# Performance work log

Measured on AMD Instinct MI355X. Metric: run time of the kernel, lower is better.

Reference implementation:

```python
import jax, jax.numpy as jnp
import numpy as np

N_CARD = 100000
N_MERCH = 50000
E = 1000000
DIN = 64
H = 128


def setup_inputs() -> dict:
    key = jax.random.key(0)
    ks = iter(jax.random.split(key, 40))

    def nrm(shape, scale=0.05):
        return jax.random.normal(next(ks), shape, jnp.float32) * scale

    inp = {}
    inp["x_card"] = jax.random.normal(next(ks), (N_CARD, DIN), jnp.float32)
    inp["x_merchant"] = jax.random.normal(next(ks), (N_MERCH, DIN), jnp.float32)
    inp["src_cm"] = jax.random.randint(next(ks), (E,), 0, N_CARD, jnp.int32)
    inp["dst_cm"] = jax.random.randint(next(ks), (E,), 0, N_MERCH, jnp.int32)
    inp["src_mc"] = jax.random.randint(next(ks), (E,), 0, N_MERCH, jnp.int32)
    inp["dst_mc"] = jax.random.randint(next(ks), (E,), 0, N_CARD, jnp.int32)
    # SAGEConv weights per layer / edge type: lin_l (on aggregated msgs, with bias), lin_r (on dst, no bias)
    inp["Wl0_cm"] = nrm((DIN, H)); inp["bl0_cm"] = jnp.zeros((H,), jnp.float32); inp["Wr0_cm"] = nrm((DIN, H))
    inp["Wl0_mc"] = nrm((DIN, H)); inp["bl0_mc"] = jnp.zeros((H,), jnp.float32); inp["Wr0_mc"] = nrm((DIN, H))
    inp["Wl1_cm"] = nrm((H, H)); inp["bl1_cm"] = jnp.zeros((H,), jnp.float32); inp["Wr1_cm"] = nrm((H, H))
    inp["Wl1_mc"] = nrm((H, H)); inp["bl1_mc"] = jnp.zeros((H,), jnp.float32); inp["Wr1_mc"] = nrm((H, H))
    # per-node-type fraud classifiers: Linear(H, H//2) -> ReLU -> Linear(H//2, 2)
    inp["cW1_card"] = nrm((H, H // 2)); inp["cb1_card"] = jnp.zeros((H // 2,), jnp.float32)
    inp["cW2_card"] = nrm((H // 2, 2)); inp["cb2_card"] = jnp.zeros((2,), jnp.float32)
    inp["cW1_merch"] = nrm((H, H // 2)); inp["cb1_merch"] = jnp.zeros((H // 2,), jnp.float32)
    inp["cW2_merch"] = nrm((H // 2, 2)); inp["cb2_merch"] = jnp.zeros((2,), jnp.float32)
    # shared risk scorer: Linear(H, H//2) -> ReLU -> Linear(H//2, 1) -> sigmoid
    inp["rW1"] = nrm((H, H // 2)); inp["rb1"] = jnp.zeros((H // 2,), jnp.float32)
    inp["rW2"] = nrm((H // 2, 1)); inp["rb2"] = jnp.zeros((1,), jnp.float32)
    return inp


def _sage(x_src, x_dst, src, dst, Wl, bl, Wr, n_dst):
    # gather neighbor features, scatter-mean by destination, then lin_l + lin_r(x_dst)
    msg = x_src[src]                                           # [E, Din]
    agg = jax.ops.segment_sum(msg, dst, num_segments=n_dst)    # [n_dst, Din]
    cnt = jax.ops.segment_sum(jnp.ones((src.shape[0],), x_src.dtype), dst, num_segments=n_dst)
    mean = agg / jnp.maximum(cnt, 1.0)[:, None]
    return mean @ Wl + bl + x_dst @ Wr


def _mlp2(x, W1, b1, W2, b2):
    return jax.nn.relu(x @ W1 + b1) @ W2 + b2


def reference(x_card, x_merchant, src_cm, dst_cm, src_mc, dst_mc,
              Wl0_cm, bl0_cm, Wr0_cm, Wl0_mc, bl0_mc, Wr0_mc,
              Wl1_cm, bl1_cm, Wr1_cm, Wl1_mc, bl1_mc, Wr1_mc,
              cW1_card, cb1_card, cW2_card, cb2_card,
              cW1_merch, cb1_merch, cW2_merch, cb2_merch,
              rW1, rb1, rW2, rb2):
    # layer 0 (eval mode: dropout is identity)
    h_m = jax.nn.relu(_sage(x_card, x_merchant, src_cm, dst_cm, Wl0_cm, bl0_cm, Wr0_cm, N_MERCH))
    h_c = jax.nn.relu(_sage(x_merchant, x_card, src_mc, dst_mc, Wl0_mc, bl0_mc, Wr0_mc, N_CARD))
    # layer 1
    h_m2 = jax.nn.relu(_sage(h_c, h_m, src_cm, dst_cm, Wl1_cm, bl1_cm, Wr1_cm, N_MERCH))
    h_c2 = jax.nn.relu(_sage(h_m, h_c, src_mc, dst_mc, Wl1_mc, bl1_mc, Wr1_mc, N_CARD))
    # heads
    pred_c = _mlp2(h_c2, cW1_card, cb1_card, cW2_card, cb2_card)      # [N_CARD, 2]
    pred_m = _mlp2(h_m2, cW1_merch, cb1_merch, cW2_merch, cb2_merch)  # [N_MERCH, 2]
    risk_c = jax.nn.sigmoid(_mlp2(h_c2, rW1, rb1, rW2, rb2))[:, 0]    # [N_CARD]
    risk_m = jax.nn.sigmoid(_mlp2(h_m2, rW1, rb1, rW2, rb2))[:, 0]    # [N_MERCH]
    return (h_c2, h_m2, pred_c, pred_m, risk_c, risk_m)
```

## Files before the change

### kernel.cpp

```cpp
#include <hip/hip_runtime.h>


typedef unsigned short u16;
typedef unsigned int u32;
typedef short bf16x8 __attribute__((ext_vector_type(8)));
typedef float f32x4 __attribute__((ext_vector_type(4)));
typedef u16 u16x4 __attribute__((ext_vector_type(4)));
typedef u16 u16x8 __attribute__((ext_vector_type(8)));

#define CAP 64
#define LDS_PAD 8

__device__ __forceinline__ float bf2f(u16 u) {
    union { u32 i; float f; } v; v.i = ((u32)u) << 16; return v.f;
}
__device__ __forceinline__ u16 f2bf(float f) {
    union { float f; u32 i; } v; v.f = f;
    u32 i = v.i;
    return (u16)((i + 0x7FFFu + ((i >> 16) & 1u)) >> 16);
}
__device__ __forceinline__ bf16x8 cvt8(const float* p) {
    bf16x8 r;
#pragma unroll
    for (int i = 0; i < 8; ++i) r[i] = (short)f2bf(p[i]);
    return r;
}

struct PackDesc { const float* src; u16* dst; int K; int Nsrc; int ntOff; };
struct PackArgs { PackDesc d[12]; };

__global__ void __launch_bounds__(256) pack_all(PackArgs pa) {
    PackDesc pd = pa.d[blockIdx.y];
    int idx = blockIdx.x * 256 + threadIdx.x;
    int j = idx & 7;
    int lane = (idx >> 3) & 63;
    int t = idx >> 9;
    int nLocal = pd.Nsrc >> 4;
    int ntl = t % nLocal;
    int kt = t / nLocal;
    if (kt >= (pd.K >> 5)) return;
    int k = kt * 32 + ((lane >> 4) << 3) + j;
    int n = ntl * 16 + (lane & 15);
    pd.dst[(((kt * 8 + pd.ntOff + ntl) * 64) + lane) * 8 + j] = f2bf(pd.src[k * pd.Nsrc + n]);
}

__global__ void __launch_bounds__(256) build_buckets(
    const int* __restrict__ src_cm, const int* __restrict__ dst_cm,
    const int* __restrict__ src_mc, const int* __restrict__ dst_mc,
    int* __restrict__ cnt_m, u32* __restrict__ bucket_m,
    int* __restrict__ cnt_c, u16* __restrict__ bucket_c, int E)
{
    int i = blockIdx.x * 256 + threadIdx.x;
    if (i < E) {
        int d = dst_cm[i];
        int slot = atomicAdd(&cnt_m[d], 1);
        if (slot < CAP) bucket_m[(size_t)d * CAP + slot] = (u32)src_cm[i];
    } else if (i < 2 * E) {
        int j = i - E;
        int d = dst_mc[j];
        int slot = atomicAdd(&cnt_c[d], 1);
        if (slot < CAP) bucket_c[(size_t)d * CAP + slot] = (u16)src_mc[j];
    }
}

template<typename IdxT, int KF, bool SRCF, bool DSTF, bool OUTF>
__global__ void __launch_bounds__(256) sage_fused(
    const void* __restrict__ Xsrc_, const IdxT* __restrict__ adj,
    const int* __restrict__ cnt,
    const u16* __restrict__ Wlp, const void* __restrict__ Xdst_,
    const u16* __restrict__ Wrp, const float* __restrict__ bias,
    void* __restrict__ out_, int M)
{
    constexpr int NV = KF / 16;
    __shared__ alignas(16) u16 lds[4][16][128 + LDS_PAD];
    const int lane = threadIdx.x & 63;
    const int wv = threadIdx.x >> 6;
    const int m0 = (blockIdx.x * 4 + wv) * 16;
    const bool active = (m0 < M);
    const int quad = lane >> 4;
    const int l15 = lane & 15;
    const int nb = quad;
    const int fl = l15;

    if (active) {
        const float* srcF = (const float*)Xsrc_;
        const u16*   srcH = (const u16*)Xsrc_;
        for (int r = 0; r < 16; ++r) {
            int node = m0 + r;
            int c = cnt[node];
            int cc = min(c, CAP);
            int sidx = (lane < cc) ? (int)adj[(size_t)node * CAP + lane] : 0;
            float inv = 1.f / (float)max(c, 1);
            float acc0[NV], acc1[NV];
#pragma unroll
            for (int i = 0; i < NV; ++i) { acc0[i] = 0.f; acc1[i] = 0.f; }
            for (int t = 0; t < cc; t += 8) {
                int k0 = t + nb;
                int k1 = t + nb + 4;
                int s0 = __shfl(sidx, k0);
                int s1 = __shfl(sidx, k1);
                bool p0 = k0 < cc;
                bool p1 = k1 < cc;
                if constexpr (SRCF) {
                    const f32x4* q0 = (const f32x4*)(srcF + (size_t)s0 * KF + fl * NV);
                    const f32x4* q1 = (const f32x4*)(srcF + (size_t)s1 * KF + fl * NV);
                    f32x4 u0 = q0[0];
                    f32x4 u1 = q1[0];
                    if constexpr (NV == 8) {
                        f32x4 w0 = q0[1];
                        f32x4 w1 = q1[1];
#pragma unroll
                        for (int i = 0; i < 4; ++i) {
                            acc0[4 + i] += p0 ? w0[i] : 0.f;
                            acc1[4 + i] += p1 ? w1[i] : 0.f;
                        }
                    }
#pragma unroll
                    for (int i = 0; i < 4; ++i) {
                        acc0[i] += p0 ? u0[i] : 0.f;
                        acc1[i] += p1 ? u1[i] : 0.f;
                    }
                } else {
                    bf16x8 u0 = *(const bf16x8*)(srcH + (size_t)s0 * KF + fl * 8);
                    bf16x8 u1 = *(const bf16x8*)(srcH + (size_t)s1 * KF + fl * 8);
#pragma unroll
                    for (int i = 0; i < 8; ++i) {
                        acc0[i] += p0 ? bf2f((u16)u0[i]) : 0.f;
                        acc1[i] += p1 ? bf2f((u16)u1[i]) : 0.f;
                    }
                }
            }
            u16 packed[NV];
#pragma unroll
            for (int i = 0; i < NV; ++i) {
                float m = acc0[i] + acc1[i];
                m += __shfl_xor(m, 16);
                m += __shfl_xor(m, 32);
                packed[i] = f2bf(m * inv);
            }
            if (nb == 0) {
                if constexpr (NV == 8) {
                    *(u16x8*)&lds[wv][r][fl * 8] = *(const u16x8*)packed;
                } else {
                    *(u16x4*)&lds[wv][r][fl * 4] = *(const u16x4*)packed;
                }
            }
        }
    }
    __syncthreads();
    if (!active) return;

    constexpr int KT = KF >> 5;
    f32x4 acc[8];
#pragma unroll
    for (int i = 0; i < 8; ++i) acc[i] = (f32x4){0.f, 0.f, 0.f, 0.f};

#pragma unroll
    for (int kt = 0; kt < KT; ++kt) {
        bf16x8 a = *reinterpret_cast<const bf16x8*>(&lds[wv][l15][kt * 32 + quad * 8]);
#pragma unroll
        for (int nt = 0; nt < 8; ++nt) {
            bf16x8 b = *reinterpret_cast<const bf16x8*>(Wlp + (size_t)(((kt * 8 + nt) * 64 + lane) * 8));
            acc[nt] = __builtin_amdgcn_mfma_f32_16x16x32_bf16(a, b, acc[nt], 0, 0, 0);
        }
    }
#pragma unroll
    for (int kt = 0; kt < KT; ++kt) {
        bf16x8 a;
        if constexpr (DSTF) a = cvt8((const float*)Xdst_ + (size_t)(m0 + l15) * KF + kt * 32 + quad * 8);
        else                a = *reinterpret_cast<const bf16x8*>((const u16*)Xdst_ + (size_t)(m0 + l15) * KF + kt * 32 + quad * 8);
#pragma unroll
        for (int nt = 0; nt < 8; ++nt) {
            bf16x8 b = *reinterpret_cast<const bf16x8*>(Wrp + (size_t)(((kt * 8 + nt) * 64 + lane) * 8));
            acc[nt] = __builtin_amdgcn_mfma_f32_16x16x32_bf16(a, b, acc[nt], 0, 0, 0);
        }
    }
#pragma unroll
    for (int nt = 0; nt < 8; ++nt) {
        int col = nt * 16 + l15;
        float bv = bias[col];
#pragma unroll
        for (int r = 0; r < 4; ++r) {
            int row = m0 + quad * 4 + r;
            float v = fmaxf(acc[nt][r] + bv, 0.f);
            if constexpr (OUTF) ((float*)out_)[(size_t)row * 128 + col] = v;
            else                ((u16*)out_)[(size_t)row * 128 + col] = f2bf(v);
        }
    }
}

__global__ void __launch_bounds__(256) head_fused(
    const float* __restrict__ X, const u16* __restrict__ W1p,
    const float* __restrict__ b1a, const float* __restrict__ b1b,
    const float* __restrict__ cW2, const float* __restrict__ cb2,
    const float* __restrict__ rW2, const float* __restrict__ rb2,
    float* __restrict__ pred, float* __restrict__ risk, int M)
{
    __shared__ alignas(16) u16 lds[4][16][128 + LDS_PAD];
    const int lane = threadIdx.x & 63;
    const int wv = threadIdx.x >> 6;
    const int m0 = (blockIdx.x * 4 + wv) * 16;
    const bool active = (m0 < M);
    const int quad = lane >> 4;
    const int l15 = lane & 15;

    if (active) {
        f32x4 acc[8];
#pragma unroll
        for (int i = 0; i < 8; ++i) acc[i] = (f32x4){0.f, 0.f, 0.f, 0.f};
#pragma unroll
        for (int kt = 0; kt < 4; ++kt) {
            bf16x8 a = cvt8(X + (size_t)(m0 + l15) * 128 + kt * 32 + quad * 8);
#pragma unroll
            for (int nt = 0; nt < 8; ++nt) {
                bf16x8 b = *reinterpret_cast<const bf16x8*>(W1p + (size_t)(((kt * 8 + nt) * 64 + lane) * 8));
                acc[nt] = __builtin_amdgcn_mfma_f32_16x16x32_bf16(a, b, acc[nt], 0, 0, 0);
            }
        }
#pragma unroll
        for (int nt = 0; nt < 8; ++nt) {
            int col = nt * 16 + l15;
            float bv = (col < 64) ? b1a[col] : b1b[col - 64];
#pragma unroll
            for (int r = 0; r < 4; ++r) {
                float v = fmaxf(acc[nt][r] + bv, 0.f);
                lds[wv][quad * 4 + r][col] = f2bf(v);
            }
        }
    }
    __syncthreads();
    if (!active) return;

    float w0 = cW2[lane * 2 + 0];
    float w1 = cW2[lane * 2 + 1];
    float w2 = rW2[lane];
    float cb0 = cb2[0], cb1v = cb2[1], rb = rb2[0];
    for (int r = 0; r < 16; ++r) {
        float t1 = bf2f(lds[wv][r][lane]);
        float t2 = bf2f(lds[wv][r][64 + lane]);
        float s0 = t1 * w0;
        float s1 = t1 * w1;
        float s2 = t2 * w2;
        for (int off = 32; off > 0; off >>= 1) {
            s0 += __shfl_xor(s0, off);
            s1 += __shfl_xor(s1, off);
            s2 += __shfl_xor(s2, off);
        }
        if (lane == 0) {
            int row = m0 + r;
            pred[(size_t)row * 2 + 0] = s0 + cb0;
            pred[(size_t)row * 2 + 1] = s1 + cb1v;
            float z = s2 + rb;
            risk[row] = 1.f / (1.f + __expf(-z));
        }
    }
}

#define OFF_CNT_M  ((size_t)0)
#define OFF_CNT_C  ((size_t)262144)
#define OFF_BKT_M  ((size_t)1  << 20)
#define OFF_BKT_C  ((size_t)14 << 20)
#define OFF_HM     ((size_t)27 << 20)
#define OFF_PACK   ((size_t)40 << 20)

extern "C" void kernel_launch(void* const* d_in, const int* in_sizes, int n_in,
                              void* d_out, int out_size, void* d_ws, size_t ws_size,
                              hipStream_t stream)
{
    const float* x_card   = (const float*)d_in[0];
    const float* x_merch  = (const float*)d_in[1];
    const int* src_cm     = (const int*)d_in[2];
    const int* dst_cm     = (const int*)d_in[3];
    const int* src_mc     = (const int*)d_in[4];
    const int* dst_mc     = (const int*)d_in[5];
    const float* Wl0_cm   = (const float*)d_in[6];
    const float* bl0_cm   = (const float*)d_in[7];
    const float* Wr0_cm   = (const float*)d_in[8];
    const float* Wl0_mc   = (const float*)d_in[9];
    const float* bl0_mc   = (const float*)d_in[10];
    const float* Wr0_mc   = (const float*)d_in[11];
    const float* Wl1_cm   = (const float*)d_in[12];
    const float* bl1_cm   = (const float*)d_in[13];
    const float* Wr1_cm   = (const float*)d_in[14];
    const float* Wl1_mc   = (const float*)d_in[15];
    const float* bl1_mc   = (const float*)d_in[16];
    const float* Wr1_mc   = (const float*)d_in[17];
    const float* cW1_card = (const float*)d_in[18];
    const float* cb1_card = (const float*)d_in[19];
    const float* cW2_card = (const float*)d_in[20];
    const float* cb2_card = (const float*)d_in[21];
    const float* cW1_mer  = (const float*)d_in[22];
    const float* cb1_mer  = (const float*)d_in[23];
    const float* cW2_mer  = (const float*)d_in[24];
    const float* cb2_mer  = (const float*)d_in[25];
    const float* rW1      = (const float*)d_in[26];
    const float* rb1      = (const float*)d_in[27];
    const float* rW2      = (const float*)d_in[28];
    const float* rb2      = (const float*)d_in[29];

    const int nCard  = in_sizes[0] / 64;
    const int nMerch = in_sizes[1] / 64;
    const int E      = in_sizes[2];

    char* ws = (char*)d_ws;
    int* cnt_m    = (int*)(ws + OFF_CNT_M);
    int* cnt_c    = (int*)(ws + OFF_CNT_C);
    u32* bucket_m = (u32*)(ws + OFF_BKT_M);
    u16* bucket_c = (u16*)(ws + OFF_BKT_C);
    u16* h_m      = (u16*)(ws + OFF_HM);
    u16* pw       = (u16*)(ws + OFF_PACK);
    u16* pWl0_cm = pw + 0 * 16384;
    u16* pWr0_cm = pw + 1 * 16384;
    u16* pWl0_mc = pw + 2 * 16384;
    u16* pWr0_mc = pw + 3 * 16384;
    u16* pWl1_cm = pw + 4 * 16384;
    u16* pWr1_cm = pw + 5 * 16384;
    u16* pWl1_mc = pw + 6 * 16384;
    u16* pWr1_mc = pw + 7 * 16384;
    u16* pHeadC  = pw + 8 * 16384;
    u16* pHeadM  = pw + 9 * 16384;

    float* out     = (float*)d_out;
    float* o_hc2   = out;
    float* o_hm2   = o_hc2 + (size_t)nCard * 128;
    float* o_predc = o_hm2 + (size_t)nMerch * 128;
    float* o_predm = o_predc + (size_t)nCard * 2;
    float* o_riskc = o_predm + (size_t)nMerch * 2;
    float* o_riskm = o_riskc + (size_t)nCard;

    hipMemsetAsync(ws, 0, OFF_CNT_C + (size_t)nCard * sizeof(int), stream);

    PackArgs pa;
    pa.d[0]  = { Wl0_cm,   pWl0_cm,  64, 128, 0 };
    pa.d[1]  = { Wr0_cm,   pWr0_cm,  64, 128, 0 };
    pa.d[2]  = { Wl0_mc,   pWl0_mc,  64, 128, 0 };
    pa.d[3]  = { Wr0_mc,   pWr0_mc,  64, 128, 0 };
    pa.d[4]  = { Wl1_cm,   pWl1_cm, 128, 128, 0 };
    pa.d[5]  = { Wr1_cm,   pWr1_cm, 128, 128, 0 };
    pa.d[6]  = { Wl1_mc,   pWl1_mc, 128, 128, 0 };
    pa.d[7]  = { Wr1_mc,   pWr1_mc, 128, 128, 0 };
    pa.d[8]  = { cW1_card, pHeadC,  128,  64, 0 };
    pa.d[9]  = { rW1,      pHeadC,  128,  64, 4 };
    pa.d[10] = { cW1_mer,  pHeadM,  128,  64, 0 };
    pa.d[11] = { rW1,      pHeadM,  128,  64, 4 };
    pack_all<<<dim3(64, 12), 256, 0, stream>>>(pa);

    build_buckets<<<(2 * E + 255) / 256, 256, 0, stream>>>(
        src_cm, dst_cm, src_mc, dst_mc, cnt_m, bucket_m, cnt_c, bucket_c, E);

    sage_fused<u32, 64, true, true, false><<<(nMerch + 63) / 64, 256, 0, stream>>>(
        x_card, bucket_m, cnt_m, pWl0_cm, x_merch, pWr0_cm, bl0_cm, h_m, nMerch);
    sage_fused<u16, 64, true, true, true><<<(nCard + 63) / 64, 256, 0, stream>>>(
        x_merch, bucket_c, cnt_c, pWl0_mc, x_card, pWr0_mc, bl0_mc, o_hc2, nCard);

    sage_fused<u32, 128, true, false, true><<<(nMerch + 63) / 64, 256, 0, stream>>>(
        o_hc2, bucket_m, cnt_m, pWl1_cm, h_m, pWr1_cm, bl1_cm, o_hm2, nMerch);
    sage_fused<u16, 128, false, true, true><<<(nCard + 63) / 64, 256, 0, stream>>>(
        h_m, bucket_c, cnt_c, pWl1_mc, o_hc2, pWr1_mc, bl1_mc, o_hc2, nCard);

    head_fused<<<(nCard + 63) / 64, 256, 0, stream>>>(
        o_hc2, pHeadC, cb1_card, rb1, cW2_card, cb2_card, rW2, rb2, o_predc, o_riskc, nCard);
    head_fused<<<(nMerch + 63) / 64, 256, 0, stream>>>(
        o_hm2, pHeadM, cb1_mer, rb1, cW2_mer, cb2_mer, rW2, rb2, o_predm, o_riskm, nMerch);
}
```

Baseline: 660.1 us.

## Partition bucket build with LDS counters and gather from bf16 shadow copies

Bucket construction is replaced by 64 blocks, each owning a slice of destination nodes. Each block scans every edge and counts its own destinations with LDS atomics, which removes the global atomics and the counter memset. Node features and the layer-0 card output are also converted to bf16 shadow buffers, so the random neighbour gathers move half the bytes. In exchange, each block rereads the full 4 MB dst array (64 passes in total), only 64 blocks run, extra conversion kernels are added, and the shadow path depends on workspace size.

```diff
diff --git a/kernel.cpp b/kernel.cpp
--- a/kernel.cpp
+++ b/kernel.cpp
@@ -10,6 +10,7 @@
 
 #define CAP 64
 #define LDS_PAD 8
+#define NPART 32
 
 __device__ __forceinline__ float bf2f(u16 u) {
     union { u32 i; float f; } v; v.i = ((u32)u) << 16; return v.f;
@@ -44,32 +45,80 @@
     pd.dst[(((kt * 8 + pd.ntOff + ntl) * 64) + lane) * 8 + j] = f2bf(pd.src[k * pd.Nsrc + n]);
 }
 
-__global__ void __launch_bounds__(256) build_buckets(
+__global__ void __launch_bounds__(256) f32_to_bf16(
+    const float* __restrict__ a, u16* __restrict__ b, int n)
+{
+    int i = (blockIdx.x * 256 + threadIdx.x) * 4;
+    if (i >= n) return;
+    f32x4 v = *reinterpret_cast<const f32x4*>(a + i);
+    u16x4 o;
+#pragma unroll
+    for (int j = 0; j < 4; ++j) o[j] = f2bf(v[j]);
+    *reinterpret_cast<u16x4*>(b + i) = o;
+}
+
+__global__ void __launch_bounds__(256) build_buckets_part(
     const int* __restrict__ src_cm, const int* __restrict__ dst_cm,
     const int* __restrict__ src_mc, const int* __restrict__ dst_mc,
     int* __restrict__ cnt_m, u32* __restrict__ bucket_m,
-    int* __restrict__ cnt_c, u16* __restrict__ bucket_c, int E)
+    int* __restrict__ cnt_c, u16* __restrict__ bucket_c,
+    int E, int nMerch, int nCard)
 {
-    int i = blockIdx.x * 256 + threadIdx.x;
-    if (i < E) {
-        int d = dst_cm[i];
-        int slot = atomicAdd(&cnt_m[d], 1);
-        if (slot < CAP) bucket_m[(size_t)d * CAP + slot] = (u32)src_cm[i];
-    } else if (i < 2 * E) {
-        int j = i - E;
-        int d = dst_mc[j];
-        int slot = atomicAdd(&cnt_c[d], 1);
-        if (slot < CAP) bucket_c[(size_t)d * CAP + slot] = (u16)src_mc[j];
-    }
-}
-
-template<typename IdxT, int KF, bool SRCF, bool DSTF, bool OUTF>
+    __shared__ int lcnt[3136];
+    const bool dirA = blockIdx.x < NPART;
+    const int part = dirA ? blockIdx.x : blockIdx.x - NPART;
+    const int nNode = dirA ? nMerch : nCard;
+    const int lo = (int)((long long)part * nNode / NPART);
+    const int hi = (int)((long long)(part + 1) * nNode / NPART);
+    const int nLoc = hi - lo;
+    const int* dst = dirA ? dst_cm : dst_mc;
+    const int* src = dirA ? src_cm : src_mc;
+
+    for (int i = threadIdx.x; i < nLoc; i += 256) lcnt[i] = 0;
+    __syncthreads();
+
+    for (int base = threadIdx.x * 4; base < E; base += 1024) {
+        if (base + 4 <= E) {
+            int4 d4 = *reinterpret_cast<const int4*>(dst + base);
+            int dv[4] = {d4.x, d4.y, d4.z, d4.w};
+#pragma unroll
+            for (int j = 0; j < 4; ++j) {
+                int d = dv[j];
+                if (d >= lo && d < hi) {
+                    int slot = atomicAdd(&lcnt[d - lo], 1);
+                    if (slot < CAP) {
+                        int s = src[base + j];
+                        if (dirA) bucket_m[(size_t)d * CAP + slot] = (u32)s;
+                        else      bucket_c[(size_t)d * CAP + slot] = (u16)s;
+                    }
+                }
+            }
+        } else {
+            for (int i = base; i < E; ++i) {
+                int d = dst[i];
+                if (d >= lo && d < hi) {
+                    int slot = atomicAdd(&lcnt[d - lo], 1);
+                    if (slot < CAP) {
+                        int s = src[i];
+                        if (dirA) bucket_m[(size_t)d * CAP + slot] = (u32)s;
+                        else      bucket_c[(size_t)d * CAP + slot] = (u16)s;
+                    }
+                }
+            }
+        }
+    }
+    __syncthreads();
+    int* gcnt = dirA ? cnt_m : cnt_c;
+    for (int i = threadIdx.x; i < nLoc; i += 256) gcnt[lo + i] = lcnt[i];
+}
+
+template<typename IdxT, int KF, bool SRCF, bool DSTF, bool OUTF, bool SHADOW>
 __global__ void __launch_bounds__(256) sage_fused(
     const void* __restrict__ Xsrc_, const IdxT* __restrict__ adj,
     const int* __restrict__ cnt,
     const u16* __restrict__ Wlp, const void* __restrict__ Xdst_,
     const u16* __restrict__ Wrp, const float* __restrict__ bias,
-    void* __restrict__ out_, int M)
+    void* __restrict__ out_, u16* __restrict__ out_bf, int M)
 {
     constexpr int NV = KF / 16;
     __shared__ alignas(16) u16 lds[4][16][128 + LDS_PAD];
@@ -121,12 +170,22 @@
                         acc1[i] += p1 ? u1[i] : 0.f;
                     }
                 } else {
-                    bf16x8 u0 = *(const bf16x8*)(srcH + (size_t)s0 * KF + fl * 8);
-                    bf16x8 u1 = *(const bf16x8*)(srcH + (size_t)s1 * KF + fl * 8);
-#pragma unroll
-                    for (int i = 0; i < 8; ++i) {
-                        acc0[i] += p0 ? bf2f((u16)u0[i]) : 0.f;
-                        acc1[i] += p1 ? bf2f((u16)u1[i]) : 0.f;
+                    if constexpr (NV == 8) {
+                        bf16x8 u0 = *(const bf16x8*)(srcH + (size_t)s0 * KF + fl * 8);
+                        bf16x8 u1 = *(const bf16x8*)(srcH + (size_t)s1 * KF + fl * 8);
+#pragma unroll
+                        for (int i = 0; i < 8; ++i) {
+                            acc0[i] += p0 ? bf2f((u16)u0[i]) : 0.f;
+                            acc1[i] += p1 ? bf2f((u16)u1[i]) : 0.f;
+                        }
+                    } else {
+                        u16x4 u0 = *(const u16x4*)(srcH + (size_t)s0 * KF + fl * 4);
+                        u16x4 u1 = *(const u16x4*)(srcH + (size_t)s1 * KF + fl * 4);
+#pragma unroll
+                        for (int i = 0; i < 4; ++i) {
+                            acc0[i] += p0 ? bf2f(u0[i]) : 0.f;
+                            acc1[i] += p1 ? bf2f(u1[i]) : 0.f;
+                        }
                     }
                 }
             }
@@ -139,11 +198,8 @@
                 packed[i] = f2bf(m * inv);
             }
             if (nb == 0) {
-                if constexpr (NV == 8) {
-                    *(u16x8*)&lds[wv][r][fl * 8] = *(const u16x8*)packed;
-                } else {
-                    *(u16x4*)&lds[wv][r][fl * 4] = *(const u16x4*)packed;
-                }
+                if constexpr (NV == 8) *(u16x8*)&lds[wv][r][fl * 8] = *(const u16x8*)packed;
+                else                   *(u16x4*)&lds[wv][r][fl * 4] = *(const u16x4*)packed;
             }
         }
     }
@@ -185,6 +241,7 @@
             float v = fmaxf(acc[nt][r] + bv, 0.f);
             if constexpr (OUTF) ((float*)out_)[(size_t)row * 128 + col] = v;
             else                ((u16*)out_)[(size_t)row * 128 + col] = f2bf(v);
+            if constexpr (SHADOW) out_bf[(size_t)row * 128 + col] = f2bf(v);
         }
     }
 }
@@ -262,6 +319,10 @@
 #define OFF_BKT_C  ((size_t)14 << 20)
 #define OFF_HM     ((size_t)27 << 20)
 #define OFF_PACK   ((size_t)40 << 20)
+#define OFF_XC     ((size_t)41 << 20)
+#define OFF_XM     ((size_t)54 << 20)
+#define OFF_HCB    ((size_t)61 << 20)
+#define WS_SHADOW_NEED ((size_t)87 << 20)
 
 extern "C" void kernel_launch(void* const* d_in, const int* in_sizes, int n_in,
                               void* d_out, int out_size, void* d_ws, size_t ws_size,
@@ -319,6 +380,11 @@
     u16* pWr1_mc = pw + 7 * 16384;
     u16* pHeadC  = pw + 8 * 16384;
     u16* pHeadM  = pw + 9 * 16384;
+    u16* xc_bf   = (u16*)(ws + OFF_XC);
+    u16* xm_bf   = (u16*)(ws + OFF_XM);
+    u16* hc_bf   = (u16*)(ws + OFF_HCB);
+
+    const bool shadow = (ws_size >= WS_SHADOW_NEED);
 
     float* out     = (float*)d_out;
     float* o_hc2   = out;
@@ -327,8 +393,6 @@
     float* o_predm = o_predc + (size_t)nCard * 2;
     float* o_riskc = o_predm + (size_t)nMerch * 2;
     float* o_riskm = o_riskc + (size_t)nCard;
-
-    hipMemsetAsync(ws, 0, OFF_CNT_C + (size_t)nCard * sizeof(int), stream);
 
     PackArgs pa;
     pa.d[0]  = { Wl0_cm,   pWl0_cm,  64, 128, 0 };
@@ -345,18 +409,33 @@
     pa.d[11] = { rW1,      pHeadM,  128,  64, 4 };
     pack_all<<<dim3(64, 12), 256, 0, stream>>>(pa);
 
-    build_buckets<<<(2 * E + 255) / 256, 256, 0, stream>>>(
-        src_cm, dst_cm, src_mc, dst_mc, cnt_m, bucket_m, cnt_c, bucket_c, E);
-
-    sage_fused<u32, 64, true, true, false><<<(nMerch + 63) / 64, 256, 0, stream>>>(
-        x_card, bucket_m, cnt_m, pWl0_cm, x_merch, pWr0_cm, bl0_cm, h_m, nMerch);
-    sage_fused<u16, 64, true, true, true><<<(nCard + 63) / 64, 256, 0, stream>>>(
-        x_merch, bucket_c, cnt_c, pWl0_mc, x_card, pWr0_mc, bl0_mc, o_hc2, nCard);
-
-    sage_fused<u32, 128, true, false, true><<<(nMerch + 63) / 64, 256, 0, stream>>>(
-        o_hc2, bucket_m, cnt_m, pWl1_cm, h_m, pWr1_cm, bl1_cm, o_hm2, nMerch);
-    sage_fused<u16, 128, false, true, true><<<(nCard + 63) / 64, 256, 0, stream>>>(
-        h_m, bucket_c, cnt_c, pWl1_mc, o_hc2, pWr1_mc, bl1_mc, o_hc2, nCard);
+    build_buckets_part<<<2 * NPART, 256, 0, stream>>>(
+        src_cm, dst_cm, src_mc, dst_mc, cnt_m, bucket_m, cnt_c, bucket_c,
+        E, nMerch, nCard);
+
+    if (shadow) {
+        f32_to_bf16<<<(nCard * 64 / 4 + 255) / 256, 256, 0, stream>>>(x_card, xc_bf, nCard * 64);
+        f32_to_bf16<<<(nMerch * 64 / 4 + 255) / 256, 256, 0, stream>>>(x_merch, xm_bf, nMerch * 64);
+
+        sage_fused<u32, 64, false, false, false, false><<<(nMerch + 63) / 64, 256, 0, stream>>>(
+            xc_bf, bucket_m, cnt_m, pWl0_cm, xm_bf, pWr0_cm, bl0_cm, h_m, nullptr, nMerch);
+        sage_fused<u16, 64, false, false, true, true><<<(nCard + 63) / 64, 256, 0, stream>>>(
+            xm_bf, bucket_c, cnt_c, pWl0_mc, xc_bf, pWr0_mc, bl0_mc, o_hc2, hc_bf, nCard);
+
+        sage_fused<u32, 128, false, false, true, false><<<(nMerch + 63) / 64, 256, 0, stream>>>(
+            hc_bf, bucket_m, cnt_m, pWl1_cm, h_m, pWr1_cm, bl1_cm, o_hm2, nullptr, nMerch);
+        sage_fused<u16, 128, false, false, true, false><<<(nCard + 63) / 64, 256, 0, stream>>>(
+            h_m, bucket_c, cnt_c, pWl1_mc, hc_bf, pWr1_mc, bl1_mc, o_hc2, nullptr, nCard);
+    } else {
+        sage_fused<u32, 64, true, true, false, false><<<(nMerch + 63) / 64, 256, 0, stream>>>(
+            x_card, bucket_m, cnt_m, pWl0_cm, x_merch, pWr0_cm, bl0_cm, h_m, nullptr, nMerch);
+        sage_fused<u16, 64, true, true, true, false><<<(nCard + 63) / 64, 256, 0, stream>>>(
+            x_merch, bucket_c, cnt_c, pWl0_mc, x_card, pWr0_mc, bl0_mc, o_hc2, nullptr, nCard);
+        sage_fused<u32, 128, true, false, true, false><<<(nMerch + 63) / 64, 256, 0, stream>>>(
+            o_hc2, bucket_m, cnt_m, pWl1_cm, h_m, pWr1_cm, bl1_cm, o_hm2, nullptr, nMerch);
+        sage_fused<u16, 128, false, true, true, false><<<(nCard + 63) / 64, 256, 0, stream>>>(
+            h_m, bucket_c, cnt_c, pWl1_mc, o_hc2, pWr1_mc, bl1_mc, o_hc2, nullptr, nCard);
+    }
 
     head_fused<<<(nCard + 63) / 64, 256, 0, stream>>>(
         o_hc2, pHeadC, cb1_card, rb1, cW2_card, cb2_card, rW2, rb2, o_predc, o_riskc, nCard);
```

New measurement: 1.899 ms. +187.7%, slower.

## Merge prep kernels, add bf16 shadow inputs, pair sage and head launches

Applied to the files above, without the earlier changes.

Folds weight packing, bucket building and bf16 conversion of the input features into one prep kernel. Bucket building is partitioned by destination range per XCD group to improve atomic locality. The card and merchant SAGE passes of each layer are merged into a single launch reading bf16 shadows, which halves gather bytes, and the two heads are merged likewise. Adjacency index loads are prefetched one row ahead. The cost is extra workspace and an extra conversion pass, and each block now rescans edges filtered by destination range.

```diff
diff --git a/kernel.cpp b/kernel.cpp
--- a/kernel.cpp
+++ b/kernel.cpp
@@ -10,6 +10,10 @@
 
 #define CAP 64
 #define LDS_PAD 8
+#define NXCD 8
+#define ECHUNK 64
+#define NBUILD (NXCD * ECHUNK * 2)
+#define NPACK  768
 
 __device__ __forceinline__ float bf2f(u16 u) {
     union { u32 i; float f; } v; v.i = ((u32)u) << 16; return v.f;
@@ -27,39 +31,205 @@
 }
 
 struct PackDesc { const float* src; u16* dst; int K; int Nsrc; int ntOff; };
-struct PackArgs { PackDesc d[12]; };
-
-__global__ void __launch_bounds__(256) pack_all(PackArgs pa) {
-    PackDesc pd = pa.d[blockIdx.y];
-    int idx = blockIdx.x * 256 + threadIdx.x;
-    int j = idx & 7;
-    int lane = (idx >> 3) & 63;
-    int t = idx >> 9;
-    int nLocal = pd.Nsrc >> 4;
-    int ntl = t % nLocal;
-    int kt = t / nLocal;
-    if (kt >= (pd.K >> 5)) return;
-    int k = kt * 32 + ((lane >> 4) << 3) + j;
-    int n = ntl * 16 + (lane & 15);
-    pd.dst[(((kt * 8 + pd.ntOff + ntl) * 64) + lane) * 8 + j] = f2bf(pd.src[k * pd.Nsrc + n]);
-}
-
-__global__ void __launch_bounds__(256) build_buckets(
-    const int* __restrict__ src_cm, const int* __restrict__ dst_cm,
-    const int* __restrict__ src_mc, const int* __restrict__ dst_mc,
-    int* __restrict__ cnt_m, u32* __restrict__ bucket_m,
-    int* __restrict__ cnt_c, u16* __restrict__ bucket_c, int E)
-{
-    int i = blockIdx.x * 256 + threadIdx.x;
-    if (i < E) {
-        int d = dst_cm[i];
-        int slot = atomicAdd(&cnt_m[d], 1);
-        if (slot < CAP) bucket_m[(size_t)d * CAP + slot] = (u32)src_cm[i];
-    } else if (i < 2 * E) {
-        int j = i - E;
-        int d = dst_mc[j];
-        int slot = atomicAdd(&cnt_c[d], 1);
-        if (slot < CAP) bucket_c[(size_t)d * CAP + slot] = (u16)src_mc[j];
+struct PrepArgs {
+    const int* src_cm; const int* dst_cm; const int* src_mc; const int* dst_mc;
+    int* cnt_m; u32* bucket_m; int* cnt_c; u16* bucket_c;
+    int E; int nMerch; int nCard;
+    const float* xc; u16* xcb; int ncBlk;
+    const float* xm; u16* xmb; int nmBlk;
+    PackDesc pd[12];
+};
+
+__global__ void __launch_bounds__(256) prep(PrepArgs a) {
+    const int b = blockIdx.x;
+    if (b < NBUILD) {
+        const int g = b & 7;
+        const int chunk = (b >> 3) & 63;
+        const bool dirA = b < (NBUILD / 2);
+        const int nNode = dirA ? a.nMerch : a.nCard;
+        const int lo = (int)((long long)g * nNode / NXCD);
+        const int hi = (int)((long long)(g + 1) * nNode / NXCD);
+        const int* dst = dirA ? a.dst_cm : a.dst_mc;
+        const int* src = dirA ? a.src_cm : a.src_mc;
+        int* cnt = dirA ? a.cnt_m : a.cnt_c;
+        const int e0 = (int)((long long)chunk * a.E / ECHUNK);
+        const int e1 = (int)((long long)(chunk + 1) * a.E / ECHUNK);
+        for (int i = e0 + threadIdx.x; i < e1; i += 256) {
+            int d = __builtin_nontemporal_load(dst + i);
+            if (d >= lo && d < hi) {
+                int slot = atomicAdd(&cnt[d], 1);
+                if (slot < CAP) {
+                    int s = __builtin_nontemporal_load(src + i);
+                    if (dirA) a.bucket_m[(size_t)d * CAP + slot] = (u32)s;
+                    else      a.bucket_c[(size_t)d * CAP + slot] = (u16)s;
+                }
+            }
+        }
+    } else if (b < NBUILD + NPACK) {
+        int e = b - NBUILD;
+        PackDesc pd = a.pd[e >> 6];
+        int idx = (e & 63) * 256 + threadIdx.x;
+        int j = idx & 7;
+        int lane = (idx >> 3) & 63;
+        int t = idx >> 9;
+        int nLocal = pd.Nsrc >> 4;
+        int ntl = t % nLocal;
+        int kt = t / nLocal;
+        if (kt >= (pd.K >> 5)) return;
+        int k = kt * 32 + ((lane >> 4) << 3) + j;
+        int n = ntl * 16 + (lane & 15);
+        pd.dst[(((kt * 8 + pd.ntOff + ntl) * 64) + lane) * 8 + j] = f2bf(pd.src[k * pd.Nsrc + n]);
+    } else {
+        int e = b - NBUILD - NPACK;
+        const float* s;
+        u16* d;
+        int n;
+        if (e < a.ncBlk) { s = a.xc; d = a.xcb; n = a.nCard * 64; }
+        else             { e -= a.ncBlk; s = a.xm; d = a.xmb; n = a.nMerch * 64; }
+        int i = (e * 256 + threadIdx.x) * 4;
+        if (i >= n) return;
+        f32x4 v = *reinterpret_cast<const f32x4*>(s + i);
+        u16x4 o;
+#pragma unroll
+        for (int j = 0; j < 4; ++j) o[j] = f2bf(v[j]);
+        *reinterpret_cast<u16x4*>(d + i) = o;
+    }
+}
+
+struct SageJob {
+    const u16* src;
+    const void* adj;
+    const int* cnt;
+    const u16* Wlp;
+    const u16* dst;
+    const u16* Wrp;
+    const float* bias;
+    float* outF;
+    u16* outH;
+    u16* outS;
+    int M;
+    int idx32;
+    int nBlk;
+};
+
+template<int KF>
+__global__ void __launch_bounds__(256) sage_pair(SageJob j0, SageJob j1) {
+    constexpr int NV = KF / 16;
+    __shared__ alignas(16) u16 lds[4][16][128 + LDS_PAD];
+    const bool second = (int)blockIdx.x >= j0.nBlk;
+    const SageJob& j = second ? j1 : j0;
+    const int bx = second ? blockIdx.x - j0.nBlk : blockIdx.x;
+    const int lane = threadIdx.x & 63;
+    const int wv = threadIdx.x >> 6;
+    const int m0 = (bx * 4 + wv) * 16;
+    const bool active = (m0 < j.M);
+    const int quad = lane >> 4;
+    const int l15 = lane & 15;
+
+    if (active) {
+        const u16* srcH = j.src;
+        const u32* adj32 = (const u32*)j.adj;
+        const u16* adj16 = (const u16*)j.adj;
+        const bool i32 = (j.idx32 != 0);
+        int cv = j.cnt[m0 + l15];
+        int cc_n = min(__shfl(cv, 0), CAP);
+        int sidx_n = 0;
+        if (lane < cc_n)
+            sidx_n = i32 ? (int)adj32[(size_t)m0 * CAP + lane]
+                         : (int)adj16[(size_t)m0 * CAP + lane];
+        for (int r = 0; r < 16; ++r) {
+            const int node = m0 + r;
+            const int cc = cc_n;
+            const int cfull = __shfl(cv, r);
+            const int sidx = sidx_n;
+            if (r < 15) {
+                cc_n = min(__shfl(cv, r + 1), CAP);
+                sidx_n = 0;
+                if (lane < cc_n)
+                    sidx_n = i32 ? (int)adj32[(size_t)(node + 1) * CAP + lane]
+                                 : (int)adj16[(size_t)(node + 1) * CAP + lane];
+            }
+            float inv = 1.f / (float)max(cfull, 1);
+            float acc0[NV], acc1[NV];
+#pragma unroll
+            for (int i = 0; i < NV; ++i) { acc0[i] = 0.f; acc1[i] = 0.f; }
+            for (int t = 0; t < cc; t += 8) {
+                int k0 = t + quad;
+                int k1 = t + quad + 4;
+                int s0 = __shfl(sidx, k0);
+                int s1 = __shfl(sidx, k1);
+                bool p0 = k0 < cc;
+                bool p1 = k1 < cc;
+                if constexpr (NV == 8) {
+                    bf16x8 u0 = *(const bf16x8*)(srcH + (size_t)s0 * KF + l15 * 8);
+                    bf16x8 u1 = *(const bf16x8*)(srcH + (size_t)s1 * KF + l15 * 8);
+#pragma unroll
+                    for (int i = 0; i < 8; ++i) {
+                        acc0[i] += p0 ? bf2f((u16)u0[i]) : 0.f;
+                        acc1[i] += p1 ? bf2f((u16)u1[i]) : 0.f;
+                    }
+                } else {
+                    u16x4 u0 = *(const u16x4*)(srcH + (size_t)s0 * KF + l15 * 4);
+                    u16x4 u1 = *(const u16x4*)(srcH + (size_t)s1 * KF + l15 * 4);
+#pragma unroll
+                    for (int i = 0; i < 4; ++i) {
+                        acc0[i] += p0 ? bf2f(u0[i]) : 0.f;
+                        acc1[i] += p1 ? bf2f(u1[i]) : 0.f;
+                    }
+                }
+            }
+            u16 packed[NV];
+#pragma unroll
+            for (int i = 0; i < NV; ++i) {
+                float m = acc0[i] + acc1[i];
+                m += __shfl_xor(m, 16);
+                m += __shfl_xor(m, 32);
+                packed[i] = f2bf(m * inv);
+            }
+            if (quad == 0) {
+                if constexpr (NV == 8) *(u16x8*)&lds[wv][r][l15 * 8] = *(const u16x8*)packed;
+                else                   *(u16x4*)&lds[wv][r][l15 * 4] = *(const u16x4*)packed;
+            }
+        }
+    }
+    __syncthreads();
+    if (!active) return;
+
+    constexpr int KT = KF >> 5;
+    f32x4 acc[8];
+#pragma unroll
+    for (int i = 0; i < 8; ++i) acc[i] = (f32x4){0.f, 0.f, 0.f, 0.f};
+
+#pragma unroll
+    for (int kt = 0; kt < KT; ++kt) {
+        bf16x8 a = *reinterpret_cast<const bf16x8*>(&lds[wv][l15][kt * 32 + quad * 8]);
+#pragma unroll
+        for (int nt = 0; nt < 8; ++nt) {
+            bf16x8 bfr = *reinterpret_cast<const bf16x8*>(j.Wlp + (size_t)(((kt * 8 + nt) * 64 + lane) * 8));
+            acc[nt] = __builtin_amdgcn_mfma_f32_16x16x32_bf16(a, bfr, acc[nt], 0, 0, 0);
+        }
+    }
+#pragma unroll
+    for (int kt = 0; kt < KT; ++kt) {
+        bf16x8 a = *reinterpret_cast<const bf16x8*>(j.dst + (size_t)(m0 + l15) * KF + kt * 32 + quad * 8);
+#pragma unroll
+        for (int nt = 0; nt < 8; ++nt) {
+            bf16x8 bfr = *reinterpret_cast<const bf16x8*>(j.Wrp + (size_t)(((kt * 8 + nt) * 64 + lane) * 8));
+            acc[nt] = __builtin_amdgcn_mfma_f32_16x16x32_bf16(a, bfr, acc[nt], 0, 0, 0);
+        }
+    }
+#pragma unroll
+    for (int nt = 0; nt < 8; ++nt) {
+        int col = nt * 16 + l15;
+        float bv = j.bias[col];
+#pragma unroll
+        for (int r = 0; r < 4; ++r) {
+            int row = m0 + quad * 4 + r;
+            float v = fmaxf(acc[nt][r] + bv, 0.f);
+            if (j.outF) j.outF[(size_t)row * 128 + col] = v;
+            if (j.outH) j.outH[(size_t)row * 128 + col] = f2bf(v);
+            if (j.outS) j.outS[(size_t)row * 128 + col] = f2bf(v);
+        }
     }
 }
 
@@ -79,8 +249,6 @@
     const bool active = (m0 < M);
     const int quad = lane >> 4;
     const int l15 = lane & 15;
-    const int nb = quad;
-    const int fl = l15;
 
     if (active) {
         const float* srcF = (const float*)Xsrc_;
@@ -95,20 +263,15 @@
 #pragma unroll
             for (int i = 0; i < NV; ++i) { acc0[i] = 0.f; acc1[i] = 0.f; }
             for (int t = 0; t < cc; t += 8) {
-                int k0 = t + nb;
-                int k1 = t + nb + 4;
-                int s0 = __shfl(sidx, k0);
-                int s1 = __shfl(sidx, k1);
-                bool p0 = k0 < cc;
-                bool p1 = k1 < cc;
+                int k0 = t + quad, k1 = t + quad + 4;
+                int s0 = __shfl(sidx, k0), s1 = __shfl(sidx, k1);
+                bool p0 = k0 < cc, p1 = k1 < cc;
                 if constexpr (SRCF) {
-                    const f32x4* q0 = (const f32x4*)(srcF + (size_t)s0 * KF + fl * NV);
-                    const f32x4* q1 = (const f32x4*)(srcF + (size_t)s1 * KF + fl * NV);
-                    f32x4 u0 = q0[0];
-                    f32x4 u1 = q1[0];
+                    const f32x4* q0 = (const f32x4*)(srcF + (size_t)s0 * KF + l15 * NV);
+                    const f32x4* q1 = (const f32x4*)(srcF + (size_t)s1 * KF + l15 * NV);
+                    f32x4 u0 = q0[0], u1 = q1[0];
                     if constexpr (NV == 8) {
-                        f32x4 w0 = q0[1];
-                        f32x4 w1 = q1[1];
+                        f32x4 w0 = q0[1], w1 = q1[1];
 #pragma unroll
                         for (int i = 0; i < 4; ++i) {
                             acc0[4 + i] += p0 ? w0[i] : 0.f;
@@ -121,12 +284,22 @@
                         acc1[i] += p1 ? u1[i] : 0.f;
                     }
                 } else {
-                    bf16x8 u0 = *(const bf16x8*)(srcH + (size_t)s0 * KF + fl * 8);
-                    bf16x8 u1 = *(const bf16x8*)(srcH + (size_t)s1 * KF + fl * 8);
-#pragma unroll
-                    for (int i = 0; i < 8; ++i) {
-                        acc0[i] += p0 ? bf2f((u16)u0[i]) : 0.f;
-                        acc1[i] += p1 ? bf2f((u16)u1[i]) : 0.f;
+                    if constexpr (NV == 8) {
+                        bf16x8 u0 = *(const bf16x8*)(srcH + (size_t)s0 * KF + l15 * 8);
+                        bf16x8 u1 = *(const bf16x8*)(srcH + (size_t)s1 * KF + l15 * 8);
+#pragma unroll
+                        for (int i = 0; i < 8; ++i) {
+                            acc0[i] += p0 ? bf2f((u16)u0[i]) : 0.f;
+                            acc1[i] += p1 ? bf2f((u16)u1[i]) : 0.f;
+                        }
+                    } else {
+                        u16x4 u0 = *(const u16x4*)(srcH + (size_t)s0 * KF + l15 * 4);
+                        u16x4 u1 = *(const u16x4*)(srcH + (size_t)s1 * KF + l15 * 4);
+#pragma unroll
+                        for (int i = 0; i < 4; ++i) {
+                            acc0[i] += p0 ? bf2f(u0[i]) : 0.f;
+                            acc1[i] += p1 ? bf2f(u1[i]) : 0.f;
+                        }
                     }
                 }
             }
@@ -138,12 +311,9 @@
                 m += __shfl_xor(m, 32);
                 packed[i] = f2bf(m * inv);
             }
-            if (nb == 0) {
-                if constexpr (NV == 8) {
-                    *(u16x8*)&lds[wv][r][fl * 8] = *(const u16x8*)packed;
-                } else {
-                    *(u16x4*)&lds[wv][r][fl * 4] = *(const u16x4*)packed;
-                }
+            if (quad == 0) {
+                if constexpr (NV == 8) *(u16x8*)&lds[wv][r][l15 * 8] = *(const u16x8*)packed;
+                else                   *(u16x4*)&lds[wv][r][l15 * 4] = *(const u16x4*)packed;
             }
         }
     }
@@ -154,7 +324,6 @@
     f32x4 acc[8];
 #pragma unroll
     for (int i = 0; i < 8; ++i) acc[i] = (f32x4){0.f, 0.f, 0.f, 0.f};
-
 #pragma unroll
     for (int kt = 0; kt < KT; ++kt) {
         bf16x8 a = *reinterpret_cast<const bf16x8*>(&lds[wv][l15][kt * 32 + quad * 8]);
@@ -189,18 +358,23 @@
     }
 }
 
-__global__ void __launch_bounds__(256) head_fused(
-    const float* __restrict__ X, const u16* __restrict__ W1p,
-    const float* __restrict__ b1a, const float* __restrict__ b1b,
-    const float* __restrict__ cW2, const float* __restrict__ cb2,
-    const float* __restrict__ rW2, const float* __restrict__ rb2,
-    float* __restrict__ pred, float* __restrict__ risk, int M)
-{
+struct HeadJob {
+    const float* X; const u16* W1p;
+    const float* b1a; const float* b1b;
+    const float* cW2; const float* cb2;
+    const float* rW2; const float* rb2;
+    float* pred; float* risk; int M; int nBlk;
+};
+
+__global__ void __launch_bounds__(256) head_pair(HeadJob h0, HeadJob h1) {
     __shared__ alignas(16) u16 lds[4][16][128 + LDS_PAD];
+    const bool second = (int)blockIdx.x >= h0.nBlk;
+    const HeadJob& h = second ? h1 : h0;
+    const int bx = second ? blockIdx.x - h0.nBlk : blockIdx.x;
     const int lane = threadIdx.x & 63;
     const int wv = threadIdx.x >> 6;
-    const int m0 = (blockIdx.x * 4 + wv) * 16;
-    const bool active = (m0 < M);
+    const int m0 = (bx * 4 + wv) * 16;
+    const bool active = (m0 < h.M);
     const int quad = lane >> 4;
     const int l15 = lane & 15;
 
@@ -210,17 +384,17 @@
         for (int i = 0; i < 8; ++i) acc[i] = (f32x4){0.f, 0.f, 0.f, 0.f};
 #pragma unroll
         for (int kt = 0; kt < 4; ++kt) {
-            bf16x8 a = cvt8(X + (size_t)(m0 + l15) * 128 + kt * 32 + quad * 8);
+            bf16x8 a = cvt8(h.X + (size_t)(m0 + l15) * 128 + kt * 32 + quad * 8);
 #pragma unroll
             for (int nt = 0; nt < 8; ++nt) {
-                bf16x8 b = *reinterpret_cast<const bf16x8*>(W1p + (size_t)(((kt * 8 + nt) * 64 + lane) * 8));
+                bf16x8 b = *reinterpret_cast<const bf16x8*>(h.W1p + (size_t)(((kt * 8 + nt) * 64 + lane) * 8));
                 acc[nt] = __builtin_amdgcn_mfma_f32_16x16x32_bf16(a, b, acc[nt], 0, 0, 0);
             }
         }
 #pragma unroll
         for (int nt = 0; nt < 8; ++nt) {
             int col = nt * 16 + l15;
-            float bv = (col < 64) ? b1a[col] : b1b[col - 64];
+            float bv = (col < 64) ? h.b1a[col] : h.b1b[col - 64];
 #pragma unroll
             for (int r = 0; r < 4; ++r) {
                 float v = fmaxf(acc[nt][r] + bv, 0.f);
@@ -231,10 +405,10 @@
     __syncthreads();
     if (!active) return;
 
-    float w0 = cW2[lane * 2 + 0];
-    float w1 = cW2[lane * 2 + 1];
-    float w2 = rW2[lane];
-    float cb0 = cb2[0], cb1v = cb2[1], rb = rb2[0];
+    float w0 = h.cW2[lane * 2 + 0];
+    float w1 = h.cW2[lane * 2 + 1];
+    float w2 = h.rW2[lane];
+    float cb0 = h.cb2[0], cb1v = h.cb2[1], rb = h.rb2[0];
     for (int r = 0; r < 16; ++r) {
         float t1 = bf2f(lds[wv][r][lane]);
         float t2 = bf2f(lds[wv][r][64 + lane]);
@@ -248,10 +422,10 @@
         }
         if (lane == 0) {
             int row = m0 + r;
-            pred[(size_t)row * 2 + 0] = s0 + cb0;
-            pred[(size_t)row * 2 + 1] = s1 + cb1v;
+            h.pred[(size_t)row * 2 + 0] = s0 + cb0;
+            h.pred[(size_t)row * 2 + 1] = s1 + cb1v;
             float z = s2 + rb;
-            risk[row] = 1.f / (1.f + __expf(-z));
+            h.risk[row] = 1.f / (1.f + __expf(-z));
         }
     }
 }
@@ -262,6 +436,10 @@
 #define OFF_BKT_C  ((size_t)14 << 20)
 #define OFF_HM     ((size_t)27 << 20)
 #define OFF_PACK   ((size_t)40 << 20)
+#define OFF_XC     ((size_t)41 << 20)
+#define OFF_XM     ((size_t)54 << 20)
+#define OFF_HCB    ((size_t)61 << 20)
+#define WS_SHADOW_NEED ((size_t)87 << 20)
 
 extern "C" void kernel_launch(void* const* d_in, const int* in_sizes, int n_in,
                               void* d_out, int out_size, void* d_ws, size_t ws_size,
@@ -319,6 +497,11 @@
     u16* pWr1_mc = pw + 7 * 16384;
     u16* pHeadC  = pw + 8 * 16384;
     u16* pHeadM  = pw + 9 * 16384;
+    u16* xc_bf   = (u16*)(ws + OFF_XC);
+    u16* xm_bf   = (u16*)(ws + OFF_XM);
+    u16* hc_bf   = (u16*)(ws + OFF_HCB);
+
+    const bool shadow = (ws_size >= WS_SHADOW_NEED);
 
     float* out     = (float*)d_out;
     float* o_hc2   = out;
@@ -330,36 +513,56 @@
 
     hipMemsetAsync(ws, 0, OFF_CNT_C + (size_t)nCard * sizeof(int), stream);
 
-    PackArgs pa;
-    pa.d[0]  = { Wl0_cm,   pWl0_cm,  64, 128, 0 };
-    pa.d[1]  = { Wr0_cm,   pWr0_cm,  64, 128, 0 };
-    pa.d[2]  = { Wl0_mc,   pWl0_mc,  64, 128, 0 };
-    pa.d[3]  = { Wr0_mc,   pWr0_mc,  64, 128, 0 };
-    pa.d[4]  = { Wl1_cm,   pWl1_cm, 128, 128, 0 };
-    pa.d[5]  = { Wr1_cm,   pWr1_cm, 128, 128, 0 };
-    pa.d[6]  = { Wl1_mc,   pWl1_mc, 128, 128, 0 };
-    pa.d[7]  = { Wr1_mc,   pWr1_mc, 128, 128, 0 };
-    pa.d[8]  = { cW1_card, pHeadC,  128,  64, 0 };
-    pa.d[9]  = { rW1,      pHeadC,  128,  64, 4 };
-    pa.d[10] = { cW1_mer,  pHeadM,  128,  64, 0 };
-    pa.d[11] = { rW1,      pHeadM,  128,  64, 4 };
-    pack_all<<<dim3(64, 12), 256, 0, stream>>>(pa);
-
-    build_buckets<<<(2 * E + 255) / 256, 256, 0, stream>>>(
-        src_cm, dst_cm, src_mc, dst_mc, cnt_m, bucket_m, cnt_c, bucket_c, E);
-
-    sage_fused<u32, 64, true, true, false><<<(nMerch + 63) / 64, 256, 0, stream>>>(
-        x_card, bucket_m, cnt_m, pWl0_cm, x_merch, pWr0_cm, bl0_cm, h_m, nMerch);
-    sage_fused<u16, 64, true, true, true><<<(nCard + 63) / 64, 256, 0, stream>>>(
-        x_merch, bucket_c, cnt_c, pWl0_mc, x_card, pWr0_mc, bl0_mc, o_hc2, nCard);
-
-    sage_fused<u32, 128, true, false, true><<<(nMerch + 63) / 64, 256, 0, stream>>>(
-        o_hc2, bucket_m, cnt_m, pWl1_cm, h_m, pWr1_cm, bl1_cm, o_hm2, nMerch);
-    sage_fused<u16, 128, false, true, true><<<(nCard + 63) / 64, 256, 0, stream>>>(
-        h_m, bucket_c, cnt_c, pWl1_mc, o_hc2, pWr1_mc, bl1_mc, o_hc2, nCard);
-
-    head_fused<<<(nCard + 63) / 64, 256, 0, stream>>>(
-        o_hc2, pHeadC, cb1_card, rb1, cW2_card, cb2_card, rW2, rb2, o_predc, o_riskc, nCard);
-    head_fused<<<(nMerch + 63) / 64, 256, 0, stream>>>(
-        o_hm2, pHeadM, cb1_mer, rb1, cW2_mer, cb2_mer, rW2, rb2, o_predm, o_riskm, nMerch);
-}
+    PrepArgs pa;
+    pa.src_cm = src_cm; pa.dst_cm = dst_cm; pa.src_mc = src_mc; pa.dst_mc = dst_mc;
+    pa.cnt_m = cnt_m; pa.bucket_m = bucket_m; pa.cnt_c = cnt_c; pa.bucket_c = bucket_c;
+    pa.E = E; pa.nMerch = nMerch; pa.nCard = nCard;
+    pa.xc = x_card;  pa.xcb = xc_bf; pa.ncBlk = shadow ? (nCard * 64 / 1024) : 0;
+    pa.xm = x_merch; pa.xmb = xm_bf; pa.nmBlk = shadow ? (nMerch * 64 / 1024) : 0;
+    pa.pd[0]  = { Wl0_cm,   pWl0_cm,  64, 128, 0 };
+    pa.pd[1]  = { Wr0_cm,   pWr0_cm,  64, 128, 0 };
+    pa.pd[2]  = { Wl0_mc,   pWl0_mc,  64, 128, 0 };
+    pa.pd[3]  = { Wr0_mc,   pWr0_mc,  64, 128, 0 };
+    pa.pd[4]  = { Wl1_cm,   pWl1_cm, 128, 128, 0 };
+    pa.pd[5]  = { Wr1_cm,   pWr1_cm, 128, 128, 0 };
+    pa.pd[6]  = { Wl1_mc,   pWl1_mc, 128, 128, 0 };
+    pa.pd[7]  = { Wr1_mc,   pWr1_mc, 128, 128, 0 };
+    pa.pd[8]  = { cW1_card, pHeadC,  128,  64, 0 };
+    pa.pd[9]  = { rW1,      pHeadC,  128,  64, 4 };
+    pa.pd[10] = { cW1_mer,  pHeadM,  128,  64, 0 };
+    pa.pd[11] = { rW1,      pHeadM,  128,  64, 4 };
+    int prepGrid = NBUILD + NPACK + pa.ncBlk + pa.nmBlk;
+    prep<<<prepGrid, 256, 0, stream>>>(pa);
+
+    const int nbM = (nMerch + 63) / 64;
+    const int nbC = (nCard + 63) / 64;
+
+    if (shadow) {
+        SageJob a0 = { xc_bf, bucket_m, cnt_m, pWl0_cm, xm_bf, pWr0_cm, bl0_cm,
+                       nullptr, h_m, nullptr, nMerch, 1, nbM };
+        SageJob a1 = { xm_bf, bucket_c, cnt_c, pWl0_mc, xc_bf, pWr0_mc, bl0_mc,
+                       o_hc2, nullptr, hc_bf, nCard, 0, nbC };
+        sage_pair<64><<<nbM + nbC, 256, 0, stream>>>(a0, a1);
+
+        SageJob b0 = { hc_bf, bucket_m, cnt_m, pWl1_cm, h_m, pWr1_cm, bl1_cm,
+                       o_hm2, nullptr, nullptr, nMerch, 1, nbM };
+        SageJob b1 = { h_m, bucket_c, cnt_c, pWl1_mc, hc_bf, pWr1_mc, bl1_mc,
+                       o_hc2, nullptr, nullptr, nCard, 0, nbC };
+        sage_pair<128><<<nbM + nbC, 256, 0, stream>>>(b0, b1);
+    } else {
+        sage_fused<u32, 64, true, true, false><<<nbM, 256, 0, stream>>>(
+            x_card, bucket_m, cnt_m, pWl0_cm, x_merch, pWr0_cm, bl0_cm, h_m, nMerch);
+        sage_fused<u16, 64, true, true, true><<<nbC, 256, 0, stream>>>(
+            x_merch, bucket_c, cnt_c, pWl0_mc, x_card, pWr0_mc, bl0_mc, o_hc2, nCard);
+        sage_fused<u32, 128, true, false, true><<<nbM, 256, 0, stream>>>(
+            o_hc2, bucket_m, cnt_m, pWl1_cm, h_m, pWr1_cm, bl1_cm, o_hm2, nMerch);
+        sage_fused<u16, 128, false, true, true><<<nbC, 256, 0, stream>>>(
+            h_m, bucket_c, cnt_c, pWl1_mc, o_hc2, pWr1_mc, bl1_mc, o_hc2, nCard);
+    }
+
+    HeadJob hc = { o_hc2, pHeadC, cb1_card, rb1, cW2_card, cb2_card, rW2, rb2,
+                   o_predc, o_riskc, nCard, nbC };
+    HeadJob hm = { o_hm2, pHeadM, cb1_mer, rb1, cW2_mer, cb2_mer, rW2, rb2,
+                   o_predm, o_riskm, nMerch, nbM };
+    head_pair<<<nbC + nbM, 256, 0, stream>>>(hc, hm);
+}
```

Result: faster. 562.1 us (-14.9%).
